# Kernel tuning notes

Measured on AMD Instinct MI355X. Metric: run time of the kernel, lower is better.

The kernel has to match this reference:

```python
import jax, jax.numpy as jnp
import numpy as np
from jax import lax

T_ITERS = 6
LN_EPS = 1e-5

def layer_norm(x, g, b):
    mu = jnp.mean(x, axis=-1, keepdims=True)
    var = jnp.var(x, axis=-1, keepdims=True)
    return (x - mu) * lax.rsqrt(var + LN_EPS) * g + b

def setup_inputs() -> dict:
    key = jax.random.key(0)
    ks = jax.random.split(key, 12)
    B, C_in, S = 8, 128, 33
    hidden = 2 * C_in          # 256
    dim = 256                  # feat_dim
    N = 64
    w = lambda k, shp, s=0.02: (jax.random.normal(k, shp, jnp.float32) * s)
    return {
        "x": jax.random.normal(ks[0], (B, C_in, S, S, S), jnp.float32),
        "templates_init": jax.random.normal(ks[1], (1, N, dim), jnp.float32),
        "conv_w": w(ks[2], (hidden, C_in, 3, 3, 3)),
        "conv_b": jnp.zeros((hidden,), jnp.float32),
        "Wq": w(ks[3], (dim, dim)),
        "Wk": w(ks[4], (hidden, dim)),
        "Wv": w(ks[5], (hidden, dim)),
        "ln_in_g": jnp.ones((hidden,), jnp.float32), "ln_in_b": jnp.zeros((hidden,), jnp.float32),
        "ln_t_g": jnp.ones((dim,), jnp.float32),    "ln_t_b": jnp.zeros((dim,), jnp.float32),
        "ln_m_g": jnp.ones((dim,), jnp.float32),    "ln_m_b": jnp.zeros((dim,), jnp.float32),
        "W1": w(ks[6], (dim, 2 * dim)), "b1": jnp.zeros((2 * dim,), jnp.float32),
        "W2": w(ks[7], (2 * dim, dim)), "b2": jnp.zeros((dim,), jnp.float32),
    }

def reference(x, templates_init, conv_w, conv_b, Wq, Wk, Wv,
              ln_in_g, ln_in_b, ln_t_g, ln_t_b, ln_m_g, ln_m_b,
              W1, b1, W2, b2):
    # project: Conv3d stride 2, no padding, + ReLU
    h = lax.conv_general_dilated(x, conv_w, window_strides=(2, 2, 2),
                                 padding='VALID',
                                 dimension_numbers=('NCDHW', 'OIDHW', 'NCDHW'))
    h = jax.nn.relu(h + conv_b[None, :, None, None, None])
    B, C, X, Y, Z = h.shape
    dim = templates_init.shape[-1]
    N = templates_init.shape[1]
    scale = dim ** (-0.5)
    tokens = h.reshape(B, C, X * Y * Z).transpose(0, 2, 1)   # (B, L, hidden)
    tokens = layer_norm(tokens, ln_in_g, ln_in_b)
    k = tokens @ Wk                                           # (B, L, dim)
    v = tokens @ Wv                                           # (B, L, dim)
    templates = jnp.broadcast_to(templates_init, (B, N, dim))
    attn = None
    for _ in range(T_ITERS):
        t_prev = templates
        t = layer_norm(templates, ln_t_g, ln_t_b)
        q = (t @ Wq) * scale                                  # (B, N, dim)
        attn_logits = jnp.einsum('bnd,bld->bln', q, k)        # (B, L, N)
        attn = jax.nn.softmax(attn_logits, axis=-1)           # competitive over N
        attn = attn + 1e-8
        attn = attn / jnp.sum(attn, axis=-2, keepdims=True)   # renormalize over L
        templates = t_prev + jnp.einsum('bld,bln->bnd', v, attn)
        m = layer_norm(templates, ln_m_g, ln_m_b)
        templates = templates + (jax.nn.gelu(m @ W1 + b1, approximate=False) @ W2 + b2)
    templates_out = templates.transpose(0, 2, 1)              # (B, dim, N)
    attn_out = attn.transpose(0, 2, 1).reshape(B, N, X, Y, Z)
    return templates_out, attn_out
```

## Files before the change

kernel.cpp:

```cpp
#include <hip/hip_runtime.h>

typedef unsigned short u16;
typedef short s16x8 __attribute__((ext_vector_type(8)));
typedef float f32x4 __attribute__((ext_vector_type(4)));
typedef float f32x4u __attribute__((ext_vector_type(4), aligned(4)));
typedef unsigned short us4 __attribute__((ext_vector_type(4)));

__device__ __forceinline__ float bf2f(u16 v) {
    return __uint_as_float(((unsigned int)v) << 16);
}
__device__ __forceinline__ u16 f2bf(float f) {
    unsigned int u = __float_as_uint(f);
    u = u + 0x7FFFu + ((u >> 16) & 1u);
    return (u16)(u >> 16);
}
__device__ __forceinline__ f32x4 mfma16(s16x8 a, s16x8 b, f32x4 c) {
    return __builtin_amdgcn_mfma_f32_16x16x32_bf16(a, b, c, 0, 0, 0);
}
#define ZERO4 f32x4{0.f, 0.f, 0.f, 0.f}

__global__ void prepack_kernel(const float* __restrict__ conv_w, const float* __restrict__ Wk,
                               const float* __restrict__ Wv, const float* __restrict__ Wq,
                               const float* __restrict__ W1, const float* __restrict__ W2,
                               u16* __restrict__ Bp, u16* __restrict__ WkvP, u16* __restrict__ WqP,
                               u16* __restrict__ W1T, u16* __restrict__ W2T)
{
    int idx = blockIdx.x * 256 + threadIdx.x;
    if (idx < 294912) {
        int n = idx / 1152, g = idx - n * 1152;
        int ic = g / 9, r = g - ic * 9;
        const float* s = conv_w + n * 3456 + ic * 27 + r * 3;
        u16* d = Bp + n * 4608 + g * 4;
        d[0] = f2bf(s[0]); d[1] = f2bf(s[1]); d[2] = f2bf(s[2]); d[3] = 0;
    } else if (idx < 425984) {
        int i = idx - 294912;
        int n = i >> 8, c = i & 255;
        WkvP[i] = f2bf((n < 256) ? Wk[c * 256 + n] : Wv[c * 256 + (n - 256)]);
    } else if (idx < 491520) {
        int i = idx - 425984;
        int n = i >> 8, c = i & 255;
        WqP[i] = f2bf(Wq[c * 256 + n]);
    } else if (idx < 622592) {
        int i = idx - 491520;
        int h = i >> 8, c = i & 255;
        W1T[i] = f2bf(W1[c * 512 + h]);
    } else if (idx < 753664) {
        int i = idx - 622592;
        int dd = i >> 9, h = i & 511;
        W2T[i] = f2bf(W2[h * 256 + dd]);
    }
}

__global__ __launch_bounds__(512, 4) void conv_fused(
    const float* __restrict__ x, const u16* __restrict__ Bp, const float* __restrict__ conv_b,
    const float* __restrict__ ln_g, const float* __restrict__ ln_b, const u16* __restrict__ WkvP,
    u16* __restrict__ kbuf, u16* __restrict__ vT)
{
    __shared__ __align__(16) char smem[38400];
    u16* slab   = (u16*)smem;
    u16* tokbf  = (u16*)smem;
    float* lnred  = (float*)(smem + 33792);
    float* lnstat = (float*)(smem + 37888);

    int blk = blockIdx.x;
    int b = blk & 7, ox = (blk >> 5) & 15, oyb = (blk >> 3) & 3;
    int tid = threadIdx.x, wid = tid >> 6, lane = tid & 63;
    int quad = lane >> 4, l15 = lane & 15;
    int nbase = wid * 32;

    f32x4 acc[4][2];
    #pragma unroll
    for (int i = 0; i < 4; ++i)
        #pragma unroll
        for (int j = 0; j < 2; ++j) acc[i][j] = ZERO4;

    const u16* bprow0 = Bp + (nbase + l15) * 4608 + quad * 8;
    const u16* bprow1 = bprow0 + 16 * 4608;

    for (int icc = 0; icc < 8; ++icc) {
        __syncthreads();
        {
            f32x4u tv[8];
            int so8[8];
            #pragma unroll
            for (int u = 0; u < 8; ++u) {
                int s = tid + u * 512;
                tv[u] = f32x4u{0.f, 0.f, 0.f, 0.f};
                so8[u] = -1;
                if (s < 3888) {
                    int row = s / 9;
                    int c = s - row * 9;
                    int icl = row / 27;
                    int rr = row - icl * 27;
                    int ixl = rr / 9;
                    int iyl = rr - ixl * 9;
                    const float* xr = x + ((size_t)((b * 128 + icc * 16 + icl) * 33)
                                           + (2 * ox + ixl)) * 1089 + (8 * oyb + iyl) * 33;
                    if (c < 8) tv[u] = *(const f32x4u*)(xr + c * 4);
                    else       tv[u].x = xr[32];
                    so8[u] = row * 36 + c * 4;
                }
            }
            #pragma unroll
            for (int u = 0; u < 8; ++u) {
                if (so8[u] >= 0) {
                    us4 w;
                    w.x = f2bf(tv[u].x); w.y = f2bf(tv[u].y);
                    w.z = f2bf(tv[u].z); w.w = f2bf(tv[u].w);
                    *(us4*)(slab + so8[u]) = w;
                }
            }
        }
        __syncthreads();

        const u16* bk0 = bprow0 + icc * 576;
        const u16* bk1 = bprow1 + icc * 576;
        s16x8 bbA[2], bbB[2];
        bbA[0] = *reinterpret_cast<const s16x8*>(bk0);
        bbA[1] = *reinterpret_cast<const s16x8*>(bk1);

#define CONV_STEP(CC, BREG)                                                     \
        {                                                                       \
            int g = (CC) * 8 + quad * 2;                                        \
            int i0 = g / 9, r9 = g - i0 * 9;                                    \
            int kx = r9 / 3, ky = r9 - kx * 3;                                  \
            int base0 = (i0 * 27 + kx * 9 + ky) * 36 + 2 * l15;                 \
            g += 1;                                                             \
            i0 = g / 9; r9 = g - i0 * 9; kx = r9 / 3; ky = r9 - kx * 3;         \
            int base1 = (i0 * 27 + kx * 9 + ky) * 36 + 2 * l15;                 \
            _Pragma("unroll")                                                   \
            for (int fm = 0; fm < 4; ++fm) {                                    \
                union { s16x8 v; ushort2 h[4]; } af;                            \
                const u16* sp0 = slab + base0 + fm * 72;                        \
                const u16* sp1 = slab + base1 + fm * 72;                        \
                af.h[0] = *(const ushort2*)(sp0);                               \
                af.h[1] = *(const ushort2*)(sp0 + 2);                           \
                af.h[2] = *(const ushort2*)(sp1);                               \
                af.h[3] = *(const ushort2*)(sp1 + 2);                           \
                acc[fm][0] = mfma16(af.v, (BREG)[0], acc[fm][0]);               \
                acc[fm][1] = mfma16(af.v, (BREG)[1], acc[fm][1]);               \
            }                                                                   \
        }

        #pragma unroll 1
        for (int c8 = 0; c8 < 18; c8 += 2) {
            bbB[0] = *reinterpret_cast<const s16x8*>(bk0 + (c8 + 1) * 32);
            bbB[1] = *reinterpret_cast<const s16x8*>(bk1 + (c8 + 1) * 32);
            CONV_STEP(c8, bbA)
            if (c8 + 2 < 18) {
                bbA[0] = *reinterpret_cast<const s16x8*>(bk0 + (c8 + 2) * 32);
                bbA[1] = *reinterpret_cast<const s16x8*>(bk1 + (c8 + 2) * 32);
            }
            CONV_STEP(c8 + 1, bbB)
        }
#undef CONV_STEP
    }
    #pragma unroll
    for (int fn = 0; fn < 2; ++fn) {
        float bias = conv_b[nbase + fn * 16 + l15];
        #pragma unroll
        for (int fm = 0; fm < 4; ++fm)
            #pragma unroll
            for (int r = 0; r < 4; ++r)
                acc[fm][fn][r] = fmaxf(acc[fm][fn][r] + bias, 0.f);
    }
    #pragma unroll
    for (int fm = 0; fm < 4; ++fm) {
        #pragma unroll
        for (int r = 0; r < 4; ++r) {
            float s = acc[fm][0][r] + acc[fm][1][r];
            float q2 = acc[fm][0][r] * acc[fm][0][r] + acc[fm][1][r] * acc[fm][1][r];
            #pragma unroll
            for (int msk = 1; msk <= 8; msk <<= 1) {
                s  += __shfl_xor(s, msk, 64);
                q2 += __shfl_xor(q2, msk, 64);
            }
            if (l15 == 0) {
                int mm = fm * 16 + quad * 4 + r;
                lnred[(wid * 64 + mm) * 2 + 0] = s;
                lnred[(wid * 64 + mm) * 2 + 1] = q2;
            }
        }
    }
    __syncthreads();
    if (tid < 64) {
        float s = 0, q2 = 0;
        #pragma unroll
        for (int w = 0; w < 8; ++w) { s += lnred[(w * 64 + tid) * 2]; q2 += lnred[(w * 64 + tid) * 2 + 1]; }
        float mu = s * (1.f / 256.f);
        float var = fmaxf(q2 * (1.f / 256.f) - mu * mu, 0.f);
        lnstat[tid * 2]     = mu;
        lnstat[tid * 2 + 1] = rsqrtf(var + 1e-5f);
    }
    __syncthreads();
    {
        float gam[2], bet[2];
        #pragma unroll
        for (int fn = 0; fn < 2; ++fn) {
            int n = nbase + fn * 16 + l15;
            gam[fn] = ln_g[n]; bet[fn] = ln_b[n];
        }
        #pragma unroll
        for (int fm = 0; fm < 4; ++fm)
            #pragma unroll
            for (int r = 0; r < 4; ++r) {
                int mm = fm * 16 + quad * 4 + r;
                float mu = lnstat[mm * 2], rs = lnstat[mm * 2 + 1];
                #pragma unroll
                for (int fn = 0; fn < 2; ++fn) {
                    int n = nbase + fn * 16 + l15;
                    tokbf[mm * 264 + n] = f2bf((acc[fm][fn][r] - mu) * rs * gam[fn] + bet[fn]);
                }
            }
    }
    __syncthreads();
    f32x4 kacc[4][4];
    #pragma unroll
    for (int i = 0; i < 4; ++i)
        #pragma unroll
        for (int j = 0; j < 4; ++j) kacc[i][j] = ZERO4;
    int n2 = wid * 64;
    const u16* wp = WkvP + (n2 + l15) * 256 + quad * 8;
    s16x8 wvA[4], wvB[4];
    #pragma unroll
    for (int fn = 0; fn < 4; ++fn) wvA[fn] = *reinterpret_cast<const s16x8*>(wp + fn * 4096);

#define KV_STEP(KK, WREG)                                                           \
    {                                                                               \
        s16x8 a2[4];                                                                \
        _Pragma("unroll")                                                           \
        for (int fm = 0; fm < 4; ++fm)                                              \
            a2[fm] = *reinterpret_cast<const s16x8*>(tokbf + (fm * 16 + l15) * 264  \
                                                     + (KK) * 32 + quad * 8);       \
        _Pragma("unroll")                                                           \
        for (int fn = 0; fn < 4; ++fn)                                              \
            _Pragma("unroll")                                                       \
            for (int fm = 0; fm < 4; ++fm)                                          \
                kacc[fm][fn] = mfma16(a2[fm], (WREG)[fn], kacc[fm][fn]);            \
    }

    #pragma unroll 1
    for (int kc = 0; kc < 8; kc += 2) {
        #pragma unroll
        for (int fn = 0; fn < 4; ++fn)
            wvB[fn] = *reinterpret_cast<const s16x8*>(wp + fn * 4096 + (kc + 1) * 32);
        KV_STEP(kc, wvA)
        if (kc + 2 < 8) {
            #pragma unroll
            for (int fn = 0; fn < 4; ++fn)
                wvA[fn] = *reinterpret_cast<const s16x8*>(wp + fn * 4096 + (kc + 2) * 32);
        }
        KV_STEP(kc + 1, wvB)
    }
#undef KV_STEP

    #pragma unroll
    for (int fm = 0; fm < 4; ++fm)
        #pragma unroll
        for (int r = 0; r < 4; ++r) {
            int l = (ox * 16 + oyb * 4 + fm) * 16 + quad * 4 + r;
            #pragma unroll
            for (int fn = 0; fn < 4; ++fn) {
                int n = n2 + fn * 16 + l15;
                u16 v = f2bf(kacc[fm][fn][r]);
                if (n < 256) kbuf[((b << 12) + l) * 256 + n] = v;
                else         vT[((b * 256 + (n - 256)) << 12) + l] = v;
            }
        }
}

__global__ __launch_bounds__(256) void kQ(
    const float* __restrict__ tinit, float* __restrict__ tpl,
    const float* __restrict__ ln_t_g, const float* __restrict__ ln_t_b,
    const u16* __restrict__ WqP, u16* __restrict__ qbuf, float* __restrict__ delta)
{
    __shared__ __align__(16) u16 mls[64 * 264];
    __shared__ float pls[64][4][2];
    __shared__ float stat[64][2];
    int b = blockIdx.x, tid = threadIdx.x;
    int m = tid >> 2, part = tid & 3;
    const float* tp = tinit + m * 256 + part * 64;
    float* tg = tpl + (b * 64 + m) * 256 + part * 64;
    float s = 0, q2 = 0;
    for (int i = 0; i < 64; ++i) {
        float v = tp[i];
        tg[i] = v;
        s += v; q2 += v * v;
    }
    pls[m][part][0] = s; pls[m][part][1] = q2;
    __syncthreads();
    if (tid < 64) {
        float ss = 0, qq = 0;
        #pragma unroll
        for (int p = 0; p < 4; ++p) { ss += pls[tid][p][0]; qq += pls[tid][p][1]; }
        float mu = ss * (1.f / 256.f);
        float var = fmaxf(qq * (1.f / 256.f) - mu * mu, 0.f);
        stat[tid][0] = mu; stat[tid][1] = rsqrtf(var + 1e-5f);
    }
    __syncthreads();
    {
        float mu = stat[m][0], rs = stat[m][1];
        for (int i = 0; i < 64; ++i) {
            int d = part * 64 + i;
            mls[m * 264 + d] = f2bf((tp[i] - mu) * rs * ln_t_g[d] + ln_t_b[d]);
        }
    }
    __syncthreads();
    int wid = tid >> 6, lane = tid & 63, quad = lane >> 4, l15 = lane & 15;
    f32x4 qa[4][4];
    #pragma unroll
    for (int i = 0; i < 4; ++i)
        #pragma unroll
        for (int j = 0; j < 4; ++j) qa[i][j] = ZERO4;
    #pragma unroll 1
    for (int kc = 0; kc < 8; ++kc) {
        s16x8 a[4];
        #pragma unroll
        for (int fm = 0; fm < 4; ++fm)
            a[fm] = *reinterpret_cast<const s16x8*>(mls + (fm * 16 + l15) * 264 + kc * 32 + quad * 8);
        #pragma unroll
        for (int fn = 0; fn < 4; ++fn) {
            s16x8 bv = *reinterpret_cast<const s16x8*>(WqP + (wid * 64 + fn * 16 + l15) * 256 + kc * 32 + quad * 8);
            #pragma unroll
            for (int fm = 0; fm < 4; ++fm)
                qa[fm][fn] = mfma16(a[fm], bv, qa[fm][fn]);
        }
    }
    #pragma unroll
    for (int fm = 0; fm < 4; ++fm)
        #pragma unroll
        for (int fn = 0; fn < 4; ++fn)
            #pragma unroll
            for (int r = 0; r < 4; ++r) {
                int mt = fm * 16 + quad * 4 + r;
                int d = wid * 64 + fn * 16 + l15;
                qbuf[(b * 64 + mt) * 256 + d] = f2bf(qa[fm][fn][r] * 0.0625f);
            }
    f32x4* dz = (f32x4*)(delta + b * 16384);
    for (int i = tid; i < 4096; i += 256) dz[i] = ZERO4;
}

__global__ __launch_bounds__(512, 2) void kA(
    const u16* __restrict__ qbuf, const u16* __restrict__ kbuf, const u16* __restrict__ vT,
    float* __restrict__ cs_part, float* __restrict__ delta, int last, u16* __restrict__ attnT)
{
    __shared__ __align__(16) u16 qls[64 * 264];
    __shared__ __align__(16) u16 atile[64 * 136];
    __shared__ float colsh[8][64];
    int b = blockIdx.x & 7, ltg = blockIdx.x >> 3;
    int tid = threadIdx.x, wid = tid >> 6, lane = tid & 63;
    int quad = lane >> 4, l15 = lane & 15;

    {
        int r = tid >> 3, c = (tid & 7) * 32;
        const u16* src = qbuf + b * 16384 + r * 256 + c;
        u16* dst = qls + r * 264 + c;
        #pragma unroll
        for (int j = 0; j < 4; ++j)
            *(int4*)(dst + j * 8) = *(const int4*)(src + j * 8);
    }
    int lrow = ltg * 128 + wid * 16;
    const u16* arow = kbuf + (size_t)((b << 12) + lrow + l15) * 256;
    s16x8 av[8];
    #pragma unroll
    for (int kc = 0; kc < 8; ++kc)
        av[kc] = *reinterpret_cast<const s16x8*>(arow + kc * 32 + quad * 8);
    __syncthreads();
    f32x4 sa[4];
    #pragma unroll
    for (int fn = 0; fn < 4; ++fn) sa[fn] = ZERO4;
    #pragma unroll
    for (int kc = 0; kc < 8; ++kc) {
        #pragma unroll
        for (int fn = 0; fn < 4; ++fn) {
            s16x8 bv = *reinterpret_cast<const s16x8*>(qls + (fn * 16 + l15) * 264 + kc * 32 + quad * 8);
            sa[fn] = mfma16(av[kc], bv, sa[fn]);
        }
    }
    float colp[4] = {0.f, 0.f, 0.f, 0.f};
    #pragma unroll
    for (int r = 0; r < 4; ++r) {
        float mx = fmaxf(fmaxf(sa[0][r], sa[1][r]), fmaxf(sa[2][r], sa[3][r]));
        #pragma unroll
        for (int msk = 1; msk <= 8; msk <<= 1) mx = fmaxf(mx, __shfl_xor(mx, msk, 64));
        float e[4], sum = 0;
        #pragma unroll
        for (int fn = 0; fn < 4; ++fn) { e[fn] = __expf(sa[fn][r] - mx); sum += e[fn]; }
        #pragma unroll
        for (int msk = 1; msk <= 8; msk <<= 1) sum += __shfl_xor(sum, msk, 64);
        float inv = 1.f / sum;
        #pragma unroll
        for (int fn = 0; fn < 4; ++fn) {
            float p = e[fn] * inv + 1e-8f;
            colp[fn] += p;
            atile[(fn * 16 + l15) * 136 + wid * 16 + quad * 4 + r] = f2bf(p);
        }
    }
    #pragma unroll
    for (int fn = 0; fn < 4; ++fn) {
        float c = colp[fn];
        c += __shfl_xor(c, 16, 64);
        c += __shfl_xor(c, 32, 64);
        if (lane < 16) colsh[wid][fn * 16 + lane] = c;
    }
    __syncthreads();
    if (tid < 64) {
        float s = 0;
        #pragma unroll
        for (int w = 0; w < 8; ++w) s += colsh[w][tid];
        cs_part[((b << 5) + ltg) * 64 + tid] = s;
    }
    {
        const u16* vrow = vT + ((size_t)(b * 256 + wid * 32 + l15) << 12) + ltg * 128 + quad * 8;
        s16x8 bv2[2][4];
        #pragma unroll
        for (int fn = 0; fn < 2; ++fn)
            #pragma unroll
            for (int kc = 0; kc < 4; ++kc)
                bv2[fn][kc] = *reinterpret_cast<const s16x8*>(vrow + (fn << 16) + kc * 32);
        f32x4 pacc[4][2];
        #pragma unroll
        for (int i = 0; i < 4; ++i)
            #pragma unroll
            for (int j = 0; j < 2; ++j) pacc[i][j] = ZERO4;
        #pragma unroll
        for (int kc = 0; kc < 4; ++kc) {
            #pragma unroll
            for (int fm = 0; fm < 4; ++fm) {
                s16x8 a = *reinterpret_cast<const s16x8*>(atile + (fm * 16 + l15) * 136 + kc * 32 + quad * 8);
                #pragma unroll
                for (int fn = 0; fn < 2; ++fn)
                    pacc[fm][fn] = mfma16(a, bv2[fn][kc], pacc[fm][fn]);
            }
        }
        #pragma unroll
        for (int fm = 0; fm < 4; ++fm)
            #pragma unroll
            for (int fn = 0; fn < 2; ++fn)
                #pragma unroll
                for (int r = 0; r < 4; ++r) {
                    int n = fm * 16 + quad * 4 + r;
                    int d = wid * 32 + fn * 16 + l15;
                    atomicAdd(&delta[(size_t)(b * 64 + n) * 256 + d], pacc[fm][fn][r]);
                }
    }
    if (last) {
        int n = tid >> 3, lo = (tid & 7) * 16;
        const u16* src = atile + n * 136 + lo;
        u16* dst = attnT + (size_t)((b * 64 + n) << 12) + ltg * 128 + lo;
        *(int4*)(dst)     = *(const int4*)(src);
        *(int4*)(dst + 8) = *(const int4*)(src + 8);
    }
}

__global__ __launch_bounds__(256) void kT(
    float* __restrict__ tpl, float* __restrict__ delta, const float* __restrict__ cs_part,
    float* __restrict__ colsum,
    const float* __restrict__ ln_m_g, const float* __restrict__ ln_m_b,
    const u16* __restrict__ W1T, const float* __restrict__ b1,
    const u16* __restrict__ W2T, const float* __restrict__ b2,
    const float* __restrict__ ln_t_g, const float* __restrict__ ln_t_b,
    const u16* __restrict__ WqP, u16* __restrict__ qbuf,
    int last, float* __restrict__ out0)
{
    __shared__ __align__(16) u16 mls[16 * 264];
    __shared__ __align__(16) u16 hid[16 * 520];
    __shared__ float pls[16][16][2];
    __shared__ float stat[16][2];
    __shared__ float lnr2[4][16][2];
    __shared__ float csh[16];
    int b = blockIdx.x & 7, mg = blockIdx.x >> 3;
    int m0 = mg * 16;
    int tid = threadIdx.x, wid = tid >> 6, lane = tid & 63;
    int quad = lane >> 4, l15 = lane & 15;
    if (tid < 16) {
        float s = 0;
        #pragma unroll
        for (int g = 0; g < 32; ++g) s += cs_part[((b << 5) + g) * 64 + m0 + tid];
        csh[tid] = 1.f / s;
        if (last) colsum[b * 64 + m0 + tid] = s;
    }
    __syncthreads();
    {
        int ml = tid >> 4, part = tid & 15;
        float cinv = csh[ml];
        float* tg = tpl + (b * 64 + m0 + ml) * 256 + part * 16;
        float* dg = delta + (size_t)(b * 64 + m0 + ml) * 256 + part * 16;
        float vbuf[16];
        float s = 0, q2 = 0;
        #pragma unroll
        for (int i = 0; i < 16; ++i) {
            float v = tg[i] + dg[i] * cinv;
            vbuf[i] = v; s += v; q2 += v * v;
        }
        if (!last) {
            f32x4* dz = (f32x4*)dg;
            #pragma unroll
            for (int i = 0; i < 4; ++i) dz[i] = ZERO4;
        }
        pls[ml][part][0] = s; pls[ml][part][1] = q2;
        __syncthreads();
        if (tid < 16) {
            float ss = 0, qq = 0;
            #pragma unroll
            for (int p = 0; p < 16; ++p) { ss += pls[tid][p][0]; qq += pls[tid][p][1]; }
            float mu = ss * (1.f / 256.f);
            float var = fmaxf(qq * (1.f / 256.f) - mu * mu, 0.f);
            stat[tid][0] = mu; stat[tid][1] = rsqrtf(var + 1e-5f);
        }
        __syncthreads();
        float mu = stat[ml][0], rs = stat[ml][1];
        #pragma unroll
        for (int i = 0; i < 16; ++i) {
            int d = part * 16 + i;
            tg[i] = vbuf[i];
            mls[ml * 264 + d] = f2bf((vbuf[i] - mu) * rs * ln_m_g[d] + ln_m_b[d]);
        }
    }
    __syncthreads();
    {
        f32x4 ha[8];
        #pragma unroll
        for (int j = 0; j < 8; ++j) ha[j] = ZERO4;
        #pragma unroll 1
        for (int kc = 0; kc < 8; ++kc) {
            s16x8 a = *reinterpret_cast<const s16x8*>(mls + l15 * 264 + kc * 32 + quad * 8);
            #pragma unroll
            for (int fn = 0; fn < 8; ++fn) {
                s16x8 bv = *reinterpret_cast<const s16x8*>(W1T + (wid * 128 + fn * 16 + l15) * 256 + kc * 32 + quad * 8);
                ha[fn] = mfma16(a, bv, ha[fn]);
            }
        }
        #pragma unroll
        for (int fn = 0; fn < 8; ++fn) {
            int nh = wid * 128 + fn * 16 + l15;
            float bb = b1[nh];
            #pragma unroll
            for (int r = 0; r < 4; ++r) {
                float v = ha[fn][r] + bb;
                v = 0.5f * v * (1.f + erff(v * 0.70710678118654752f));
                hid[(quad * 4 + r) * 520 + nh] = f2bf(v);
            }
        }
    }
    __syncthreads();
    {
        f32x4 oa[4];
        #pragma unroll
        for (int j = 0; j < 4; ++j) oa[j] = ZERO4;
        #pragma unroll 1
        for (int kc = 0; kc < 16; ++kc) {
            s16x8 a = *reinterpret_cast<const s16x8*>(hid + l15 * 520 + kc * 32 + quad * 8);
            #pragma unroll
            for (int fn = 0; fn < 4; ++fn) {
                s16x8 bv = *reinterpret_cast<const s16x8*>(W2T + (wid * 64 + fn * 16 + l15) * 512 + kc * 32 + quad * 8);
                oa[fn] = mfma16(a, bv, oa[fn]);
            }
        }
        #pragma unroll
        for (int fn = 0; fn < 4; ++fn) {
            int d = wid * 64 + fn * 16 + l15;
            float bb = b2[d];
            #pragma unroll
            for (int r = 0; r < 4; ++r) {
                int mm = quad * 4 + r;
                oa[fn][r] += bb + tpl[(b * 64 + m0 + mm) * 256 + d];
            }
        }
        #pragma unroll
        for (int r = 0; r < 4; ++r) {
            float s = oa[0][r] + oa[1][r] + oa[2][r] + oa[3][r];
            float q2 = oa[0][r] * oa[0][r] + oa[1][r] * oa[1][r]
                     + oa[2][r] * oa[2][r] + oa[3][r] * oa[3][r];
            #pragma unroll
            for (int msk = 1; msk <= 8; msk <<= 1) {
                s  += __shfl_xor(s, msk, 64);
                q2 += __shfl_xor(q2, msk, 64);
            }
            if (l15 == 0) {
                lnr2[wid][quad * 4 + r][0] = s;
                lnr2[wid][quad * 4 + r][1] = q2;
            }
        }
        __syncthreads();
        if (tid < 16) {
            float ss = 0, qq = 0;
            #pragma unroll
            for (int w = 0; w < 4; ++w) { ss += lnr2[w][tid][0]; qq += lnr2[w][tid][1]; }
            float mu = ss * (1.f / 256.f);
            float var = fmaxf(qq * (1.f / 256.f) - mu * mu, 0.f);
            stat[tid][0] = mu; stat[tid][1] = rsqrtf(var + 1e-5f);
        }
        __syncthreads();
        #pragma unroll
        for (int fn = 0; fn < 4; ++fn) {
            int d = wid * 64 + fn * 16 + l15;
            float gg = last ? 0.f : ln_t_g[d];
            float bt = last ? 0.f : ln_t_b[d];
            #pragma unroll
            for (int r = 0; r < 4; ++r) {
                int mm = quad * 4 + r;
                float v = oa[fn][r];
                tpl[(b * 64 + m0 + mm) * 256 + d] = v;
                if (last) {
                    out0[(b * 256 + d) * 64 + m0 + mm] = v;
                } else {
                    mls[mm * 264 + d] = f2bf((v - stat[mm][0]) * stat[mm][1] * gg + bt);
                }
            }
        }
    }
    if (!last) {
        __syncthreads();
        f32x4 qa[4];
        #pragma unroll
        for (int j = 0; j < 4; ++j) qa[j] = ZERO4;
        #pragma unroll 1
        for (int kc = 0; kc < 8; ++kc) {
            s16x8 a = *reinterpret_cast<const s16x8*>(mls + l15 * 264 + kc * 32 + quad * 8);
            #pragma unroll
            for (int fn = 0; fn < 4; ++fn) {
                s16x8 bv = *reinterpret_cast<const s16x8*>(WqP + (wid * 64 + fn * 16 + l15) * 256 + kc * 32 + quad * 8);
                qa[fn] = mfma16(a, bv, qa[fn]);
            }
        }
        #pragma unroll
        for (int fn = 0; fn < 4; ++fn)
            #pragma unroll
            for (int r = 0; r < 4; ++r) {
                int mt = m0 + quad * 4 + r;
                int d = wid * 64 + fn * 16 + l15;
                qbuf[(b * 64 + mt) * 256 + d] = f2bf(qa[fn][r] * 0.0625f);
            }
    }
}

__global__ void kE(const u16* __restrict__ attnT, const float* __restrict__ colsum,
                   float* __restrict__ out1)
{
    int blk = blockIdx.x;
    int b = blk & 7, r8 = blk >> 3;
    int e = (b << 18) + (r8 << 10) + threadIdx.x * 4;
    int n = (e >> 12) & 63;
    float ci = 1.f / colsum[b * 64 + n];
    const u16* s = attnT + e;
    f32x4 o;
    o.x = bf2f(s[0]) * ci; o.y = bf2f(s[1]) * ci;
    o.z = bf2f(s[2]) * ci; o.w = bf2f(s[3]) * ci;
    *(f32x4*)(out1 + e) = o;
}

extern "C" void kernel_launch(void* const* d_in, const int* in_sizes, int n_in,
                              void* d_out, int out_size, void* d_ws, size_t ws_size,
                              hipStream_t stream)
{
    const float* x       = (const float*)d_in[0];
    const float* tinit   = (const float*)d_in[1];
    const float* conv_w  = (const float*)d_in[2];
    const float* conv_b  = (const float*)d_in[3];
    const float* Wq      = (const float*)d_in[4];
    const float* Wk      = (const float*)d_in[5];
    const float* Wv      = (const float*)d_in[6];
    const float* ln_in_g = (const float*)d_in[7];
    const float* ln_in_b = (const float*)d_in[8];
    const float* ln_t_g  = (const float*)d_in[9];
    const float* ln_t_b  = (const float*)d_in[10];
    const float* ln_m_g  = (const float*)d_in[11];
    const float* ln_m_b  = (const float*)d_in[12];
    const float* W1      = (const float*)d_in[13];
    const float* b1      = (const float*)d_in[14];
    const float* W2      = (const float*)d_in[15];
    const float* b2      = (const float*)d_in[16];

    char* ws = (char*)d_ws;
    u16* Bp       = (u16*)(ws + 0);
    u16* WkvP     = (u16*)(ws + 2359296);
    u16* WqP      = (u16*)(ws + 2621440);
    u16* W1T      = (u16*)(ws + 2752512);
    u16* W2T      = (u16*)(ws + 3014656);
    u16* kbuf     = (u16*)(ws + 3276800);
    u16* vT       = (u16*)(ws + 20054016);
    u16* qbuf     = (u16*)(ws + 36831232);
    u16* attnT    = (u16*)(ws + 37093376);
    float* colsum = (float*)(ws + 41287680);
    float* tpl    = (float*)(ws + 41289728);
    float* delta  = (float*)(ws + 41814016);
    float* cs_part= (float*)(ws + 42338304);

    float* out0 = (float*)d_out;
    float* out1 = out0 + 131072;

    prepack_kernel<<<2944, 256, 0, stream>>>(conv_w, Wk, Wv, Wq, W1, W2, Bp, WkvP, WqP, W1T, W2T);
    conv_fused<<<512, 512, 0, stream>>>(x, Bp, conv_b, ln_in_g, ln_in_b, WkvP, kbuf, vT);
    kQ<<<8, 256, 0, stream>>>(tinit, tpl, ln_t_g, ln_t_b, WqP, qbuf, delta);
    for (int it = 0; it < 6; ++it) {
        int last = (it == 5) ? 1 : 0;
        kA<<<256, 512, 0, stream>>>(qbuf, kbuf, vT, cs_part, delta, last, attnT);
        kT<<<32, 256, 0, stream>>>(tpl, delta, cs_part, colsum, ln_m_g, ln_m_b, W1T, b1, W2T, b2,
                                   ln_t_g, ln_t_b, WqP, qbuf, last, out0);
    }
    kE<<<2048, 256, 0, stream>>>(attnT, colsum, out1);
}
```

Before: 749.1 us.

## Double-buffer conv input slab, hoist V loads in kA, widen kT to 512 threads

The conv kernel now double-buffers its bf16 input slab in LDS, issuing the global loads for the next input-channel chunk before the MFMA loop on the current chunk, so memory latency overlaps with compute. In kA, the V operand loads move ahead of the barrier to start earlier. kT runs with 512 threads instead of 256, halving per-wave work in its small GEMMs and layer norms. The double buffer roughly doubles conv LDS use, which may cut occupancy below the launch_bounds target of 4 blocks, and the prefetched values take extra registers.

```diff
diff --git a/kernel.cpp b/kernel.cpp
--- a/kernel.cpp
+++ b/kernel.cpp
@@ -56,11 +56,12 @@
     const float* __restrict__ ln_g, const float* __restrict__ ln_b, const u16* __restrict__ WkvP,
     u16* __restrict__ kbuf, u16* __restrict__ vT)
 {
-    __shared__ __align__(16) char smem[38400];
-    u16* slab   = (u16*)smem;
+    __shared__ __align__(16) char smem[66816];
+    u16* slab0  = (u16*)smem;
+    u16* slab1  = (u16*)(smem + 31104);
     u16* tokbf  = (u16*)smem;
-    float* lnred  = (float*)(smem + 33792);
-    float* lnstat = (float*)(smem + 37888);
+    float* lnred  = (float*)(smem + 62208);
+    float* lnstat = (float*)(smem + 66304);
 
     int blk = blockIdx.x;
     int b = blk & 7, ox = (blk >> 5) & 15, oyb = (blk >> 3) & 3;
@@ -77,41 +78,60 @@
     const u16* bprow0 = Bp + (nbase + l15) * 4608 + quad * 8;
     const u16* bprow1 = bprow0 + 16 * 4608;
 
+    const float* xp[8]; int so8[8]; unsigned wmask = 0;
+    #pragma unroll
+    for (int u = 0; u < 8; ++u) {
+        int s = tid + u * 512;
+        so8[u] = -1; xp[u] = x;
+        if (s < 3888) {
+            int row = s / 9;
+            int c = s - row * 9;
+            int icl = row / 27;
+            int rr = row - icl * 27;
+            int ixl = rr / 9;
+            int iyl = rr - ixl * 9;
+            const float* xr = x + ((size_t)((b * 128 + icl) * 33) + (2 * ox + ixl)) * 1089
+                              + (8 * oyb + iyl) * 33;
+            if (c < 8) { xp[u] = xr + c * 4; wmask |= (1u << u); }
+            else       { xp[u] = xr + 32; }
+            so8[u] = row * 36 + c * 4;
+        }
+    }
+    const size_t ICST = 16ull * 35937;
+
+    f32x4u tv[8];
+#define LOADX(ICC)                                                          \
+    {                                                                       \
+        _Pragma("unroll")                                                   \
+        for (int u = 0; u < 8; ++u) {                                       \
+            if (so8[u] >= 0) {                                              \
+                const float* p = xp[u] + (size_t)(ICC) * ICST;              \
+                if ((wmask >> u) & 1u) tv[u] = *(const f32x4u*)p;           \
+                else                   tv[u] = f32x4u{p[0], 0.f, 0.f, 0.f}; \
+            }                                                               \
+        }                                                                   \
+    }
+#define STOREX(DST)                                                         \
+    {                                                                       \
+        _Pragma("unroll")                                                   \
+        for (int u = 0; u < 8; ++u) {                                       \
+            if (so8[u] >= 0) {                                              \
+                us4 w;                                                      \
+                w.x = f2bf(tv[u].x); w.y = f2bf(tv[u].y);                   \
+                w.z = f2bf(tv[u].z); w.w = f2bf(tv[u].w);                   \
+                *(us4*)((DST) + so8[u]) = w;                                \
+            }                                                               \
+        }                                                                   \
+    }
+
+    LOADX(0)
+    STOREX(slab0)
+    __syncthreads();
+
     for (int icc = 0; icc < 8; ++icc) {
-        __syncthreads();
-        {
-            f32x4u tv[8];
-            int so8[8];
-            #pragma unroll
-            for (int u = 0; u < 8; ++u) {
-                int s = tid + u * 512;
-                tv[u] = f32x4u{0.f, 0.f, 0.f, 0.f};
-                so8[u] = -1;
-                if (s < 3888) {
-                    int row = s / 9;
-                    int c = s - row * 9;
-                    int icl = row / 27;
-                    int rr = row - icl * 27;
-                    int ixl = rr / 9;
-                    int iyl = rr - ixl * 9;
-                    const float* xr = x + ((size_t)((b * 128 + icc * 16 + icl) * 33)
-                                           + (2 * ox + ixl)) * 1089 + (8 * oyb + iyl) * 33;
-                    if (c < 8) tv[u] = *(const f32x4u*)(xr + c * 4);
-                    else       tv[u].x = xr[32];
-                    so8[u] = row * 36 + c * 4;
-                }
-            }
-            #pragma unroll
-            for (int u = 0; u < 8; ++u) {
-                if (so8[u] >= 0) {
-                    us4 w;
-                    w.x = f2bf(tv[u].x); w.y = f2bf(tv[u].y);
-                    w.z = f2bf(tv[u].z); w.w = f2bf(tv[u].w);
-                    *(us4*)(slab + so8[u]) = w;
-                }
-            }
-        }
-        __syncthreads();
+        const u16* cur = (icc & 1) ? slab1 : slab0;
+        u16* nxt = (icc & 1) ? slab0 : slab1;
+        if (icc < 7) LOADX(icc + 1)
 
         const u16* bk0 = bprow0 + icc * 576;
         const u16* bk1 = bprow1 + icc * 576;
@@ -131,8 +151,8 @@
             _Pragma("unroll")                                                   \
             for (int fm = 0; fm < 4; ++fm) {                                    \
                 union { s16x8 v; ushort2 h[4]; } af;                            \
-                const u16* sp0 = slab + base0 + fm * 72;                        \
-                const u16* sp1 = slab + base1 + fm * 72;                        \
+                const u16* sp0 = cur + base0 + fm * 72;                         \
+                const u16* sp1 = cur + base1 + fm * 72;                         \
                 af.h[0] = *(const ushort2*)(sp0);                               \
                 af.h[1] = *(const ushort2*)(sp0 + 2);                           \
                 af.h[2] = *(const ushort2*)(sp1);                               \
@@ -154,7 +174,12 @@
             CONV_STEP(c8 + 1, bbB)
         }
 #undef CONV_STEP
-    }
+        if (icc < 7) STOREX(nxt)
+        __syncthreads();
+    }
+#undef LOADX
+#undef STOREX
+
     #pragma unroll
     for (int fn = 0; fn < 2; ++fn) {
         float bias = conv_b[nbase + fn * 16 + l15];
@@ -365,6 +390,13 @@
     #pragma unroll
     for (int kc = 0; kc < 8; ++kc)
         av[kc] = *reinterpret_cast<const s16x8*>(arow + kc * 32 + quad * 8);
+    const u16* vrow = vT + ((size_t)(b * 256 + wid * 32 + l15) << 12) + ltg * 128 + quad * 8;
+    s16x8 bv2[2][4];
+    #pragma unroll
+    for (int fn = 0; fn < 2; ++fn)
+        #pragma unroll
+        for (int kc = 0; kc < 4; ++kc)
+            bv2[fn][kc] = *reinterpret_cast<const s16x8*>(vrow + (fn << 16) + kc * 32);
     __syncthreads();
     f32x4 sa[4];
     #pragma unroll
@@ -411,13 +443,6 @@
         cs_part[((b << 5) + ltg) * 64 + tid] = s;
     }
     {
-        const u16* vrow = vT + ((size_t)(b * 256 + wid * 32 + l15) << 12) + ltg * 128 + quad * 8;
-        s16x8 bv2[2][4];
-        #pragma unroll
-        for (int fn = 0; fn < 2; ++fn)
-            #pragma unroll
-            for (int kc = 0; kc < 4; ++kc)
-                bv2[fn][kc] = *reinterpret_cast<const s16x8*>(vrow + (fn << 16) + kc * 32);
         f32x4 pacc[4][2];
         #pragma unroll
         for (int i = 0; i < 4; ++i)
@@ -453,7 +478,7 @@
     }
 }
 
-__global__ __launch_bounds__(256) void kT(
+__global__ __launch_bounds__(512) void kT(
     float* __restrict__ tpl, float* __restrict__ delta, const float* __restrict__ cs_part,
     float* __restrict__ colsum,
     const float* __restrict__ ln_m_g, const float* __restrict__ ln_m_b,
@@ -465,9 +490,9 @@
 {
     __shared__ __align__(16) u16 mls[16 * 264];
     __shared__ __align__(16) u16 hid[16 * 520];
-    __shared__ float pls[16][16][2];
+    __shared__ float pls[16][32][2];
     __shared__ float stat[16][2];
-    __shared__ float lnr2[4][16][2];
+    __shared__ float lnr2[8][16][2];
     __shared__ float csh[16];
     int b = blockIdx.x & 7, mg = blockIdx.x >> 3;
     int m0 = mg * 16;
@@ -482,28 +507,27 @@
     }
     __syncthreads();
     {
-        int ml = tid >> 4, part = tid & 15;
+        int ml = tid >> 5, part = tid & 31;
         float cinv = csh[ml];
-        float* tg = tpl + (b * 64 + m0 + ml) * 256 + part * 16;
-        float* dg = delta + (size_t)(b * 64 + m0 + ml) * 256 + part * 16;
-        float vbuf[16];
+        float* tg = tpl + (b * 64 + m0 + ml) * 256 + part * 8;
+        float* dg = delta + (size_t)(b * 64 + m0 + ml) * 256 + part * 8;
+        float vbuf[8];
         float s = 0, q2 = 0;
         #pragma unroll
-        for (int i = 0; i < 16; ++i) {
+        for (int i = 0; i < 8; ++i) {
             float v = tg[i] + dg[i] * cinv;
             vbuf[i] = v; s += v; q2 += v * v;
         }
         if (!last) {
             f32x4* dz = (f32x4*)dg;
-            #pragma unroll
-            for (int i = 0; i < 4; ++i) dz[i] = ZERO4;
+            dz[0] = ZERO4; dz[1] = ZERO4;
         }
         pls[ml][part][0] = s; pls[ml][part][1] = q2;
         __syncthreads();
         if (tid < 16) {
             float ss = 0, qq = 0;
             #pragma unroll
-            for (int p = 0; p < 16; ++p) { ss += pls[tid][p][0]; qq += pls[tid][p][1]; }
+            for (int p = 0; p < 32; ++p) { ss += pls[tid][p][0]; qq += pls[tid][p][1]; }
             float mu = ss * (1.f / 256.f);
             float var = fmaxf(qq * (1.f / 256.f) - mu * mu, 0.f);
             stat[tid][0] = mu; stat[tid][1] = rsqrtf(var + 1e-5f);
@@ -511,29 +535,29 @@
         __syncthreads();
         float mu = stat[ml][0], rs = stat[ml][1];
         #pragma unroll
-        for (int i = 0; i < 16; ++i) {
-            int d = part * 16 + i;
+        for (int i = 0; i < 8; ++i) {
+            int d = part * 8 + i;
             tg[i] = vbuf[i];
             mls[ml * 264 + d] = f2bf((vbuf[i] - mu) * rs * ln_m_g[d] + ln_m_b[d]);
         }
     }
     __syncthreads();
     {
-        f32x4 ha[8];
-        #pragma unroll
-        for (int j = 0; j < 8; ++j) ha[j] = ZERO4;
+        f32x4 ha[4];
+        #pragma unroll
+        for (int j = 0; j < 4; ++j) ha[j] = ZERO4;
         #pragma unroll 1
         for (int kc = 0; kc < 8; ++kc) {
             s16x8 a = *reinterpret_cast<const s16x8*>(mls + l15 * 264 + kc * 32 + quad * 8);
             #pragma unroll
-            for (int fn = 0; fn < 8; ++fn) {
-                s16x8 bv = *reinterpret_cast<const s16x8*>(W1T + (wid * 128 + fn * 16 + l15) * 256 + kc * 32 + quad * 8);
+            for (int fn = 0; fn < 4; ++fn) {
+                s16x8 bv = *reinterpret_cast<const s16x8*>(W1T + (wid * 64 + fn * 16 + l15) * 256 + kc * 32 + quad * 8);
                 ha[fn] = mfma16(a, bv, ha[fn]);
             }
         }
         #pragma unroll
-        for (int fn = 0; fn < 8; ++fn) {
-            int nh = wid * 128 + fn * 16 + l15;
+        for (int fn = 0; fn < 4; ++fn) {
+            int nh = wid * 64 + fn * 16 + l15;
             float bb = b1[nh];
             #pragma unroll
             for (int r = 0; r < 4; ++r) {
@@ -545,21 +569,20 @@
     }
     __syncthreads();
     {
-        f32x4 oa[4];
-        #pragma unroll
-        for (int j = 0; j < 4; ++j) oa[j] = ZERO4;
+        f32x4 oa[2];
+        oa[0] = ZERO4; oa[1] = ZERO4;
         #pragma unroll 1
         for (int kc = 0; kc < 16; ++kc) {
             s16x8 a = *reinterpret_cast<const s16x8*>(hid + l15 * 520 + kc * 32 + quad * 8);
             #pragma unroll
-            for (int fn = 0; fn < 4; ++fn) {
-                s16x8 bv = *reinterpret_cast<const s16x8*>(W2T + (wid * 64 + fn * 16 + l15) * 512 + kc * 32 + quad * 8);
+            for (int fn = 0; fn < 2; ++fn) {
+                s16x8 bv = *reinterpret_cast<const s16x8*>(W2T + (wid * 32 + fn * 16 + l15) * 512 + kc * 32 + quad * 8);
                 oa[fn] = mfma16(a, bv, oa[fn]);
             }
         }
         #pragma unroll
-        for (int fn = 0; fn < 4; ++fn) {
-            int d = wid * 64 + fn * 16 + l15;
+        for (int fn = 0; fn < 2; ++fn) {
+            int d = wid * 32 + fn * 16 + l15;
             float bb = b2[d];
             #pragma unroll
             for (int r = 0; r < 4; ++r) {
@@ -569,9 +592,8 @@
         }
         #pragma unroll
         for (int r = 0; r < 4; ++r) {
-            float s = oa[0][r] + oa[1][r] + oa[2][r] + oa[3][r];
-            float q2 = oa[0][r] * oa[0][r] + oa[1][r] * oa[1][r]
-                     + oa[2][r] * oa[2][r] + oa[3][r] * oa[3][r];
+            float s = oa[0][r] + oa[1][r];
+            float q2 = oa[0][r] * oa[0][r] + oa[1][r] * oa[1][r];
             #pragma unroll
             for (int msk = 1; msk <= 8; msk <<= 1) {
                 s  += __shfl_xor(s, msk, 64);
@@ -586,15 +608,15 @@
         if (tid < 16) {
             float ss = 0, qq = 0;
             #pragma unroll
-            for (int w = 0; w < 4; ++w) { ss += lnr2[w][tid][0]; qq += lnr2[w][tid][1]; }
+            for (int w = 0; w < 8; ++w) { ss += lnr2[w][tid][0]; qq += lnr2[w][tid][1]; }
             float mu = ss * (1.f / 256.f);
             float var = fmaxf(qq * (1.f / 256.f) - mu * mu, 0.f);
             stat[tid][0] = mu; stat[tid][1] = rsqrtf(var + 1e-5f);
         }
         __syncthreads();
         #pragma unroll
-        for (int fn = 0; fn < 4; ++fn) {
-            int d = wid * 64 + fn * 16 + l15;
+        for (int fn = 0; fn < 2; ++fn) {
+            int d = wid * 32 + fn * 16 + l15;
             float gg = last ? 0.f : ln_t_g[d];
             float bt = last ? 0.f : ln_t_b[d];
             #pragma unroll
@@ -612,24 +634,23 @@
     }
     if (!last) {
         __syncthreads();
-        f32x4 qa[4];
-        #pragma unroll
-        for (int j = 0; j < 4; ++j) qa[j] = ZERO4;
+        f32x4 qa[2];
+        qa[0] = ZERO4; qa[1] = ZERO4;
         #pragma unroll 1
         for (int kc = 0; kc < 8; ++kc) {
             s16x8 a = *reinterpret_cast<const s16x8*>(mls + l15 * 264 + kc * 32 + quad * 8);
             #pragma unroll
-            for (int fn = 0; fn < 4; ++fn) {
-                s16x8 bv = *reinterpret_cast<const s16x8*>(WqP + (wid * 64 + fn * 16 + l15) * 256 + kc * 32 + quad * 8);
+            for (int fn = 0; fn < 2; ++fn) {
+                s16x8 bv = *reinterpret_cast<const s16x8*>(WqP + (wid * 32 + fn * 16 + l15) * 256 + kc * 32 + quad * 8);
                 qa[fn] = mfma16(a, bv, qa[fn]);
             }
         }
         #pragma unroll
-        for (int fn = 0; fn < 4; ++fn)
+        for (int fn = 0; fn < 2; ++fn)
             #pragma unroll
             for (int r = 0; r < 4; ++r) {
                 int mt = m0 + quad * 4 + r;
-                int d = wid * 64 + fn * 16 + l15;
+                int d = wid * 32 + fn * 16 + l15;
                 qbuf[(b * 64 + mt) * 256 + d] = f2bf(qa[fn][r] * 0.0625f);
             }
     }
@@ -696,7 +717,7 @@
     for (int it = 0; it < 6; ++it) {
         int last = (it == 5) ? 1 : 0;
         kA<<<256, 512, 0, stream>>>(qbuf, kbuf, vT, cs_part, delta, last, attnT);
-        kT<<<32, 256, 0, stream>>>(tpl, delta, cs_part, colsum, ln_m_g, ln_m_b, W1T, b1, W2T, b2,
+        kT<<<32, 512, 0, stream>>>(tpl, delta, cs_part, colsum, ln_m_g, ln_m_b, W1T, b1, W2T, b2,
                                    ln_t_g, ln_t_b, WqP, qbuf, last, out0);
     }
     kE<<<2048, 256, 0, stream>>>(attnT, colsum, out1);
```

New measurement: 716.8 us. 4.3% less time.
